# Optimization experiments

Hardware: AMD Instinct MI355X
Metric: run time of the kernel (lower is better)

## Reference

```python
import jax, jax.numpy as jnp
import numpy as np

FP8_MAX = 448.0  # max finite value of float8_e4m3fn


def setup_inputs() -> dict:
    key = jax.random.key(0)
    k1, k2, k3 = jax.random.split(key, 3)
    B, S, D_IN, D_OUT = 2, 4096, 2048, 8192
    x = jax.random.normal(k1, (B, S, D_IN), dtype=jnp.float32)
    # Weight is stored pre-quantized in fp8 (per-tensor scale), layout (in, out)
    w_fp32 = jax.random.normal(k2, (D_IN, D_OUT), dtype=jnp.float32) * 0.02
    weight_scale = jnp.float32(jnp.max(jnp.abs(w_fp32)) / FP8_MAX)
    weight = jnp.clip(w_fp32 / weight_scale, -FP8_MAX, FP8_MAX).astype(jnp.float8_e4m3fn)
    input_scale = jnp.float32(0.05)  # static per-tensor activation scale
    bias = jax.random.normal(k3, (D_OUT,), dtype=jnp.float32)
    return {"x": x, "weight": weight, "weight_scale": weight_scale,
            "input_scale": input_scale, "bias": bias}


def reference(x, weight, weight_scale, input_scale, bias):
    # static_quantize_e4m3_per_tensor: q = cast_fp8(clip(x / s)), returns (q, s)
    q = jnp.clip(x / input_scale, -FP8_MAX, FP8_MAX).astype(jnp.float8_e4m3fn)
    q2d = q.reshape(-1, q.shape[-1]).astype(jnp.float32)  # [B*S, D_in]
    w = weight.astype(jnp.float32)                         # [D_in, D_out]
    # cublas_scaled_mm: (q @ w) * scale_a * scale_b, out in x.dtype
    out = jnp.matmul(q2d, w) * (input_scale * weight_scale)
    out = out.astype(x.dtype) + bias.astype(x.dtype)
    return out.reshape(x.shape[:-1] + (out.shape[-1],))
```

## Files before the change

### kernel.cpp

```cpp
#include <hip/hip_runtime.h>

typedef __attribute__((ext_vector_type(4)))  float floatx4;
typedef __attribute__((ext_vector_type(16))) float floatx16;
typedef __attribute__((ext_vector_type(8)))  int   intx8;

__device__ __forceinline__ unsigned int pack4_fp8(float f0, float f1, float f2, float f3) {
    int v = __builtin_amdgcn_cvt_pk_fp8_f32(f0, f1, 0, false);
    v = __builtin_amdgcn_cvt_pk_fp8_f32(f2, f3, v, true);
    return (unsigned int)v;
}

__device__ __forceinline__ void gload16(const unsigned char* g, unsigned char* l) {
    __builtin_amdgcn_global_load_lds(
        (const __attribute__((address_space(1))) unsigned int*)g,
        (__attribute__((address_space(3))) unsigned int*)l, 16, 0, 0);
}

__global__ void detect_kernel(const unsigned int* __restrict__ W, int* __restrict__ flag) {
    __shared__ int ok[2];
    if (threadIdx.x == 0) { ok[0] = 1; ok[1] = 1; }
    __syncthreads();
    int f32ok = 1, bf16ok = 1;
#pragma unroll
    for (int i = 0; i < 16; ++i) {
        unsigned int w = W[threadIdx.x * 16 + i];
        if (w & 0x000FFFFFu) f32ok = 0;
        if (w & 0x000F000Fu) bf16ok = 0;
    }
    if (!f32ok)  atomicAnd(&ok[0], 0);
    if (!bf16ok) atomicAnd(&ok[1], 0);
    __syncthreads();
    if (threadIdx.x == 0) *flag = ok[0] ? 2 : (ok[1] ? 1 : 0);
}

__global__ void quant_kernel(const float* __restrict__ x,
                             unsigned int* __restrict__ q,
                             const float* __restrict__ iscale, int n8) {
    int i = blockIdx.x * blockDim.x + threadIdx.x;
    if (i >= n8) return;
    float s = iscale[0];
    const float4* xv = (const float4*)x;
    float4 a = xv[2 * i];
    float4 b = xv[2 * i + 1];
    float v[8] = {a.x, a.y, a.z, a.w, b.x, b.y, b.z, b.w};
#pragma unroll
    for (int j = 0; j < 8; ++j) {
        float t = v[j] / s;
        v[j] = fminf(fmaxf(t, -448.0f), 448.0f);
    }
    q[2 * i]     = pack4_fp8(v[0], v[1], v[2], v[3]);
    q[2 * i + 1] = pack4_fp8(v[4], v[5], v[6], v[7]);
}

template <int MODE>
__device__ __forceinline__ void ingest_body(const unsigned char* __restrict__ W,
                                            unsigned char* __restrict__ Wt,
                                            int K, int N,
                                            unsigned char (*tile)[68]) {
    const int k0 = blockIdx.y * 64;
    const int n0 = blockIdx.x * 64;
    const int t = threadIdx.x;
    const int kr = t >> 2;
    const int cg = (t & 3) * 16;
    const size_t eidx = (size_t)(k0 + kr) * N + (n0 + cg);

    unsigned int w4[4];
    if constexpr (MODE == 0) {
        uint4 v = *(const uint4*)(W + eidx);
        w4[0] = v.x; w4[1] = v.y; w4[2] = v.z; w4[3] = v.w;
    } else if constexpr (MODE == 1) {
        const uint4* p = (const uint4*)((const unsigned short*)W + eidx);
        uint4 A0 = p[0], A1 = p[1];
        unsigned int uw[8] = {A0.x, A0.y, A0.z, A0.w, A1.x, A1.y, A1.z, A1.w};
#pragma unroll
        for (int g = 0; g < 4; ++g) {
            float f0 = __uint_as_float((uw[2 * g] & 0xFFFFu) << 16);
            float f1 = __uint_as_float((uw[2 * g] >> 16) << 16);
            float f2 = __uint_as_float((uw[2 * g + 1] & 0xFFFFu) << 16);
            float f3 = __uint_as_float((uw[2 * g + 1] >> 16) << 16);
            w4[g] = pack4_fp8(f0, f1, f2, f3);
        }
    } else {
        const float4* p = (const float4*)((const float*)W + eidx);
#pragma unroll
        for (int g = 0; g < 4; ++g) {
            float4 f = p[g];
            w4[g] = pack4_fp8(f.x, f.y, f.z, f.w);
        }
    }
#pragma unroll
    for (int g = 0; g < 4; ++g)
        *(unsigned int*)&tile[kr][cg + 4 * g] = w4[g];
    __syncthreads();

    const int nr = t >> 2;
    const int kg = (t & 3) * 16;
    uint4 o;
    unsigned int w[4];
#pragma unroll
    for (int g = 0; g < 4; ++g) {
        unsigned int b0 = tile[kg + g * 4 + 0][nr];
        unsigned int b1 = tile[kg + g * 4 + 1][nr];
        unsigned int b2 = tile[kg + g * 4 + 2][nr];
        unsigned int b3 = tile[kg + g * 4 + 3][nr];
        w[g] = b0 | (b1 << 8) | (b2 << 16) | (b3 << 24);
    }
    o.x = w[0]; o.y = w[1]; o.z = w[2]; o.w = w[3];
    *(uint4*)(Wt + (size_t)(n0 + nr) * K + k0 + kg) = o;
}

__global__ void ingest_kernel(const unsigned char* __restrict__ W,
                              unsigned char* __restrict__ Wt,
                              const int* __restrict__ flag, int K, int N) {
    __shared__ __align__(16) unsigned char tile[64][68];
    const int mode = *flag;
    if (mode == 0)      ingest_body<0>(W, Wt, K, N, tile);
    else if (mode == 1) ingest_body<1>(W, Wt, K, N, tile);
    else                ingest_body<2>(W, Wt, K, N, tile);
}

__global__ __launch_bounds__(512, 2) void gemm_mxfp8_kernel(
    const unsigned char* __restrict__ A,
    const unsigned char* __restrict__ Bt,
    float* __restrict__ C,
    const float* __restrict__ bias,
    const float* __restrict__ wscale,
    const float* __restrict__ iscale,
    int M, int N, int K) {
    __shared__ __align__(16) unsigned char As[2 * 32768];
    __shared__ __align__(16) unsigned char Bs[2 * 32768];

    const int tid  = threadIdx.x;
    const int lane = tid & 63;
    const int wv   = tid >> 6;
    const int wm   = wv >> 2;
    const int wn   = wv & 3;
    const int r16  = lane & 15;
    const int cq   = lane >> 4;

    const int bm = blockIdx.y * 256;
    const int bn = blockIdx.x * 256;

    const unsigned char* ga[4];
    const unsigned char* gb[4];
    int lo[4];
#pragma unroll
    for (int j = 0; j < 4; ++j) {
        const int u   = wv * 4 + j;
        const int rb  = u >> 1;
        const int rg  = u & 1;
        const int row = rb * 16 + r16;
        const int col = cq * 32 + rg * 16;
        ga[j] = A  + (size_t)(bm + row) * K + col;
        gb[j] = Bt + (size_t)(bn + row) * K + col;
        lo[j] = u * 1024;
    }

    floatx16 acc[4][2] = {};
    const int NT = K >> 7;

    const int labase = ((lane >> 4) & 1) * 2048 + (lane & 15) * 16 + (lane >> 5) * 256;

#pragma unroll
    for (int j = 0; j < 4; ++j) {
        gload16(ga[j], &As[lo[j]]);
        gload16(gb[j], &Bs[lo[j]]);
        ga[j] += 128; gb[j] += 128;
    }
    if (NT > 1) {
#pragma unroll
        for (int j = 0; j < 4; ++j) {
            gload16(gb[j], &Bs[32768 + lo[j]]);
            gb[j] += 128;
        }
        asm volatile("s_waitcnt vmcnt(4)" ::: "memory");
    } else {
        asm volatile("s_waitcnt vmcnt(0)" ::: "memory");
    }
    __builtin_amdgcn_s_barrier();
    __builtin_amdgcn_sched_barrier(0);

    union U8 { intx8 v; uint4 q[2]; };

#define READ_FRAG(dst, p)                                           \
    do {                                                            \
        U8 _u;                                                      \
        _u.q[0] = *(const uint4*)(p);                               \
        _u.q[1] = *(const uint4*)((p) + 1024);                      \
        (dst) = _u.v;                                               \
    } while (0)

#define MFMA4(afA, afB, mA, mB, b0_, b1_)                                   \
    do {                                                                    \
        __builtin_amdgcn_s_setprio(1);                                      \
        acc[mA][0] = __builtin_amdgcn_mfma_scale_f32_32x32x64_f8f6f4(       \
            afA, b0_, acc[mA][0], 0, 0, 0, 0x7F7F7F7F, 0, 0x7F7F7F7F);      \
        acc[mA][1] = __builtin_amdgcn_mfma_scale_f32_32x32x64_f8f6f4(       \
            afA, b1_, acc[mA][1], 0, 0, 0, 0x7F7F7F7F, 0, 0x7F7F7F7F);      \
        acc[mB][0] = __builtin_amdgcn_mfma_scale_f32_32x32x64_f8f6f4(       \
            afB, b0_, acc[mB][0], 0, 0, 0, 0x7F7F7F7F, 0, 0x7F7F7F7F);      \
        acc[mB][1] = __builtin_amdgcn_mfma_scale_f32_32x32x64_f8f6f4(       \
            afB, b1_, acc[mB][1], 0, 0, 0, 0x7F7F7F7F, 0, 0x7F7F7F7F);      \
        __builtin_amdgcn_s_setprio(0);                                      \
    } while (0)

#define PHASE_WAIT()                                             \
    do {                                                         \
        __builtin_amdgcn_s_barrier();                            \
        asm volatile("s_waitcnt lgkmcnt(0)" ::: "memory");       \
        __builtin_amdgcn_sched_barrier(0);                       \
    } while (0)

    for (int kt = 0; kt < NT; ++kt) {
        const unsigned char* Ab = &As[(kt & 1) * 32768];
        const unsigned char* Bb = &Bs[(kt & 1) * 32768];
        unsigned char* An  = &As[((kt + 1) & 1) * 32768];
        unsigned char* Bn2 = &Bs[(kt & 1) * 32768];
        const bool pfA = (kt + 1 < NT);
        const bool pfB = (kt + 2 < NT);

        const unsigned char* aB = Ab + labase;
        const unsigned char* bB = Bb + labase;
        intx8 b00, b01, b10, b11, af0, af1;

        READ_FRAG(b00, bB + (wn * 4 + 0) * 2048);
        READ_FRAG(b01, bB + (wn * 4 + 2) * 2048);
        READ_FRAG(af0, aB + (wm * 8 + 0) * 2048);
        READ_FRAG(af1, aB + (wm * 8 + 2) * 2048);
        if (pfA) {
            gload16(ga[0], An + lo[0]); gload16(ga[1], An + lo[1]);
            ga[0] += 128; ga[1] += 128;
        }
        PHASE_WAIT();
        MFMA4(af0, af1, 0, 1, b00, b01);
        __builtin_amdgcn_s_barrier();

        READ_FRAG(b10, bB + (wn * 4 + 0) * 2048 + 512);
        READ_FRAG(b11, bB + (wn * 4 + 2) * 2048 + 512);
        READ_FRAG(af0, aB + (wm * 8 + 4) * 2048);
        READ_FRAG(af1, aB + (wm * 8 + 6) * 2048);
        if (pfA) {
            gload16(ga[2], An + lo[2]); gload16(ga[3], An + lo[3]);
            ga[2] += 128; ga[3] += 128;
        }
        PHASE_WAIT();
        MFMA4(af0, af1, 2, 3, b00, b01);
        __builtin_amdgcn_s_barrier();

        READ_FRAG(af0, aB + (wm * 8 + 0) * 2048 + 512);
        READ_FRAG(af1, aB + (wm * 8 + 2) * 2048 + 512);
        if (pfB) {
            gload16(gb[0], Bn2 + lo[0]); gload16(gb[1], Bn2 + lo[1]);
            gb[0] += 128; gb[1] += 128;
        }
        PHASE_WAIT();
        MFMA4(af0, af1, 0, 1, b10, b11);
        __builtin_amdgcn_s_barrier();

        READ_FRAG(af0, aB + (wm * 8 + 4) * 2048 + 512);
        READ_FRAG(af1, aB + (wm * 8 + 6) * 2048 + 512);
        if (pfB) {
            gload16(gb[2], Bn2 + lo[2]); gload16(gb[3], Bn2 + lo[3]);
            gb[2] += 128; gb[3] += 128;
        }
        PHASE_WAIT();
        MFMA4(af0, af1, 2, 3, b10, b11);
        if (pfB) {
            asm volatile("s_waitcnt vmcnt(4)" ::: "memory");
        } else {
            asm volatile("s_waitcnt vmcnt(0)" ::: "memory");
        }
        __builtin_amdgcn_s_barrier();
        __builtin_amdgcn_sched_barrier(0);
    }
    (void)M; (void)r16; (void)cq;
#undef READ_FRAG
#undef MFMA4
#undef PHASE_WAIT

    const float scale = iscale[0] * wscale[0];
    const int colb = bn + wn * 64 + (lane & 31);
    const float bv0 = bias[colb];
    const float bv1 = bias[colb + 32];
    const int rowb = bm + wm * 128 + 4 * (lane >> 5);
#pragma unroll
    for (int mb = 0; mb < 4; ++mb) {
#pragma unroll
        for (int r = 0; r < 16; ++r) {
            const int row = rowb + mb * 32 + (r & 3) + 8 * (r >> 2);
            float* cp = C + (size_t)row * N + colb;
            cp[0]  = acc[mb][0][r] * scale + bv0;
            cp[32] = acc[mb][1][r] * scale + bv1;
        }
    }
}

extern "C" void kernel_launch(void* const* d_in, const int* in_sizes, int n_in,
                              void* d_out, int out_size, void* d_ws, size_t ws_size,
                              hipStream_t stream) {
    const float* x          = (const float*)d_in[0];
    const unsigned char* w  = (const unsigned char*)d_in[1];
    const float* wscale     = (const float*)d_in[2];
    const float* iscale     = (const float*)d_in[3];
    const float* bias       = (const float*)d_in[4];
    float* out              = (float*)d_out;

    const int D_OUT = in_sizes[4];
    const int D_IN  = in_sizes[1] / D_OUT;
    const int M     = in_sizes[0] / D_IN;

    int* flag         = (int*)d_ws;
    unsigned char* q  = (unsigned char*)d_ws + 256;
    unsigned char* wt = q + (size_t)M * D_IN;

    detect_kernel<<<1, 256, 0, stream>>>((const unsigned int*)w, flag);
    const int n8 = (M * D_IN) / 8;
    quant_kernel<<<(n8 + 255) / 256, 256, 0, stream>>>(x, (unsigned int*)q, iscale, n8);
    dim3 tg(D_OUT / 64, D_IN / 64);
    ingest_kernel<<<tg, 256, 0, stream>>>(w, wt, flag, D_IN, D_OUT);
    gemm_mxfp8_kernel<<<dim3(D_OUT / 256, M / 256), 512, 0, stream>>>(
        q, wt, out, bias, wscale, iscale, M, D_OUT, D_IN);
}
```

Baseline: 507.4 us.

## Fuse prep kernels into one launch and halve GEMM K-tile depth

The detect, quantize and weight-ingest kernels are merged into one prep kernel. Blocks are split between activation quantization and weight transposition, and each ingest block now repeats the format detection itself, which removes two launches and the flag round-trip. The GEMM K-step drops from 128 to 64 bytes, halving shared-memory buffers to 64KB and cutting each iteration to two MFMA phases. This lowers LDS use and may raise occupancy, at the cost of twice as many barriers and loop iterations per unit of K.

Measured after the change: 503.5 us. Within noise of the previous version (-0.8%).

```diff
diff --git a/kernel.cpp b/kernel.cpp
--- a/kernel.cpp
+++ b/kernel.cpp
@@ -16,49 +16,11 @@
         (__attribute__((address_space(3))) unsigned int*)l, 16, 0, 0);
 }
 
-__global__ void detect_kernel(const unsigned int* __restrict__ W, int* __restrict__ flag) {
-    __shared__ int ok[2];
-    if (threadIdx.x == 0) { ok[0] = 1; ok[1] = 1; }
-    __syncthreads();
-    int f32ok = 1, bf16ok = 1;
-#pragma unroll
-    for (int i = 0; i < 16; ++i) {
-        unsigned int w = W[threadIdx.x * 16 + i];
-        if (w & 0x000FFFFFu) f32ok = 0;
-        if (w & 0x000F000Fu) bf16ok = 0;
-    }
-    if (!f32ok)  atomicAnd(&ok[0], 0);
-    if (!bf16ok) atomicAnd(&ok[1], 0);
-    __syncthreads();
-    if (threadIdx.x == 0) *flag = ok[0] ? 2 : (ok[1] ? 1 : 0);
-}
-
-__global__ void quant_kernel(const float* __restrict__ x,
-                             unsigned int* __restrict__ q,
-                             const float* __restrict__ iscale, int n8) {
-    int i = blockIdx.x * blockDim.x + threadIdx.x;
-    if (i >= n8) return;
-    float s = iscale[0];
-    const float4* xv = (const float4*)x;
-    float4 a = xv[2 * i];
-    float4 b = xv[2 * i + 1];
-    float v[8] = {a.x, a.y, a.z, a.w, b.x, b.y, b.z, b.w};
-#pragma unroll
-    for (int j = 0; j < 8; ++j) {
-        float t = v[j] / s;
-        v[j] = fminf(fmaxf(t, -448.0f), 448.0f);
-    }
-    q[2 * i]     = pack4_fp8(v[0], v[1], v[2], v[3]);
-    q[2 * i + 1] = pack4_fp8(v[4], v[5], v[6], v[7]);
-}
-
 template <int MODE>
 __device__ __forceinline__ void ingest_body(const unsigned char* __restrict__ W,
                                             unsigned char* __restrict__ Wt,
-                                            int K, int N,
+                                            int K, int N, int k0, int n0,
                                             unsigned char (*tile)[68]) {
-    const int k0 = blockIdx.y * 64;
-    const int n0 = blockIdx.x * 64;
     const int t = threadIdx.x;
     const int kr = t >> 2;
     const int cg = (t & 3) * 16;
@@ -109,14 +71,53 @@
     *(uint4*)(Wt + (size_t)(n0 + nr) * K + k0 + kg) = o;
 }
 
-__global__ void ingest_kernel(const unsigned char* __restrict__ W,
-                              unsigned char* __restrict__ Wt,
-                              const int* __restrict__ flag, int K, int N) {
+__global__ __launch_bounds__(256) void prep_kernel(
+    const float* __restrict__ x, unsigned int* __restrict__ q,
+    const float* __restrict__ iscale, int n8, int nbq,
+    const unsigned char* __restrict__ W, unsigned char* __restrict__ Wt,
+    int K, int N) {
+    __shared__ int ok[2];
     __shared__ __align__(16) unsigned char tile[64][68];
-    const int mode = *flag;
-    if (mode == 0)      ingest_body<0>(W, Wt, K, N, tile);
-    else if (mode == 1) ingest_body<1>(W, Wt, K, N, tile);
-    else                ingest_body<2>(W, Wt, K, N, tile);
+
+    if ((int)blockIdx.x < nbq) {
+        int i = blockIdx.x * 256 + threadIdx.x;
+        if (i >= n8) return;
+        float s = iscale[0];
+        const float4* xv = (const float4*)x;
+        float4 a = xv[2 * i];
+        float4 b = xv[2 * i + 1];
+        float v[8] = {a.x, a.y, a.z, a.w, b.x, b.y, b.z, b.w};
+#pragma unroll
+        for (int j = 0; j < 8; ++j) {
+            float t = v[j] / s;
+            v[j] = fminf(fmaxf(t, -448.0f), 448.0f);
+        }
+        q[2 * i]     = pack4_fp8(v[0], v[1], v[2], v[3]);
+        q[2 * i + 1] = pack4_fp8(v[4], v[5], v[6], v[7]);
+        return;
+    }
+
+    if (threadIdx.x == 0) { ok[0] = 1; ok[1] = 1; }
+    __syncthreads();
+    int f32ok = 1, bf16ok = 1;
+#pragma unroll
+    for (int i = 0; i < 16; ++i) {
+        unsigned int w = ((const unsigned int*)W)[threadIdx.x * 16 + i];
+        if (w & 0x000FFFFFu) f32ok = 0;
+        if (w & 0x000F000Fu) bf16ok = 0;
+    }
+    if (!f32ok)  atomicAnd(&ok[0], 0);
+    if (!bf16ok) atomicAnd(&ok[1], 0);
+    __syncthreads();
+    const int mode = ok[0] ? 2 : (ok[1] ? 1 : 0);
+
+    const int bx = blockIdx.x - nbq;
+    const int ntn = N >> 6;
+    const int n0 = (bx % ntn) * 64;
+    const int k0 = (bx / ntn) * 64;
+    if (mode == 0)      ingest_body<0>(W, Wt, K, N, k0, n0, tile);
+    else if (mode == 1) ingest_body<1>(W, Wt, K, N, k0, n0, tile);
+    else                ingest_body<2>(W, Wt, K, N, k0, n0, tile);
 }
 
 __global__ __launch_bounds__(512, 2) void gemm_mxfp8_kernel(
@@ -127,8 +128,8 @@
     const float* __restrict__ wscale,
     const float* __restrict__ iscale,
     int M, int N, int K) {
-    __shared__ __align__(16) unsigned char As[2 * 32768];
-    __shared__ __align__(16) unsigned char Bs[2 * 32768];
+    __shared__ __align__(16) unsigned char As[2 * 16384];
+    __shared__ __align__(16) unsigned char Bs[2 * 16384];
 
     const int tid  = threadIdx.x;
     const int lane = tid & 63;
@@ -141,39 +142,37 @@
     const int bm = blockIdx.y * 256;
     const int bn = blockIdx.x * 256;
 
-    const unsigned char* ga[4];
-    const unsigned char* gb[4];
-    int lo[4];
-#pragma unroll
-    for (int j = 0; j < 4; ++j) {
-        const int u   = wv * 4 + j;
-        const int rb  = u >> 1;
-        const int rg  = u & 1;
-        const int row = rb * 16 + r16;
-        const int col = cq * 32 + rg * 16;
+    const unsigned char* ga[2];
+    const unsigned char* gb[2];
+    int lo[2];
+#pragma unroll
+    for (int j = 0; j < 2; ++j) {
+        const int u   = wv * 2 + j;
+        const int row = u * 16 + r16;
+        const int col = cq * 16;
         ga[j] = A  + (size_t)(bm + row) * K + col;
         gb[j] = Bt + (size_t)(bn + row) * K + col;
         lo[j] = u * 1024;
     }
 
     floatx16 acc[4][2] = {};
-    const int NT = K >> 7;
-
-    const int labase = ((lane >> 4) & 1) * 2048 + (lane & 15) * 16 + (lane >> 5) * 256;
-
-#pragma unroll
-    for (int j = 0; j < 4; ++j) {
+    const int NT = K >> 6;
+
+    const int labase = ((lane >> 4) & 1) * 1024 + (lane & 15) * 16 + (lane >> 5) * 512;
+
+#pragma unroll
+    for (int j = 0; j < 2; ++j) {
         gload16(ga[j], &As[lo[j]]);
         gload16(gb[j], &Bs[lo[j]]);
-        ga[j] += 128; gb[j] += 128;
+        ga[j] += 64; gb[j] += 64;
     }
     if (NT > 1) {
 #pragma unroll
-        for (int j = 0; j < 4; ++j) {
-            gload16(gb[j], &Bs[32768 + lo[j]]);
-            gb[j] += 128;
-        }
-        asm volatile("s_waitcnt vmcnt(4)" ::: "memory");
+        for (int j = 0; j < 2; ++j) {
+            gload16(gb[j], &Bs[16384 + lo[j]]);
+            gb[j] += 64;
+        }
+        asm volatile("s_waitcnt vmcnt(2)" ::: "memory");
     } else {
         asm volatile("s_waitcnt vmcnt(0)" ::: "memory");
     }
@@ -186,7 +185,7 @@
     do {                                                            \
         U8 _u;                                                      \
         _u.q[0] = *(const uint4*)(p);                               \
-        _u.q[1] = *(const uint4*)((p) + 1024);                      \
+        _u.q[1] = *(const uint4*)((p) + 256);                       \
         (dst) = _u.v;                                               \
     } while (0)
 
@@ -212,68 +211,46 @@
     } while (0)
 
     for (int kt = 0; kt < NT; ++kt) {
-        const unsigned char* Ab = &As[(kt & 1) * 32768];
-        const unsigned char* Bb = &Bs[(kt & 1) * 32768];
-        unsigned char* An  = &As[((kt + 1) & 1) * 32768];
-        unsigned char* Bn2 = &Bs[(kt & 1) * 32768];
+        const unsigned char* Ab = &As[(kt & 1) * 16384];
+        const unsigned char* Bb = &Bs[(kt & 1) * 16384];
+        unsigned char* An  = &As[((kt + 1) & 1) * 16384];
+        unsigned char* Bn2 = &Bs[(kt & 1) * 16384];
         const bool pfA = (kt + 1 < NT);
         const bool pfB = (kt + 2 < NT);
 
         const unsigned char* aB = Ab + labase;
         const unsigned char* bB = Bb + labase;
-        intx8 b00, b01, b10, b11, af0, af1;
-
-        READ_FRAG(b00, bB + (wn * 4 + 0) * 2048);
-        READ_FRAG(b01, bB + (wn * 4 + 2) * 2048);
-        READ_FRAG(af0, aB + (wm * 8 + 0) * 2048);
-        READ_FRAG(af1, aB + (wm * 8 + 2) * 2048);
+        intx8 b0, b1, a0, a1;
+
+        READ_FRAG(b0, bB + (wn * 2 + 0) * 2048);
+        READ_FRAG(b1, bB + (wn * 2 + 1) * 2048);
+        READ_FRAG(a0, aB + (wm * 4 + 0) * 2048);
+        READ_FRAG(a1, aB + (wm * 4 + 1) * 2048);
         if (pfA) {
             gload16(ga[0], An + lo[0]); gload16(ga[1], An + lo[1]);
-            ga[0] += 128; ga[1] += 128;
+            ga[0] += 64; ga[1] += 64;
         }
         PHASE_WAIT();
-        MFMA4(af0, af1, 0, 1, b00, b01);
+        MFMA4(a0, a1, 0, 1, b0, b1);
         __builtin_amdgcn_s_barrier();
 
-        READ_FRAG(b10, bB + (wn * 4 + 0) * 2048 + 512);
-        READ_FRAG(b11, bB + (wn * 4 + 2) * 2048 + 512);
-        READ_FRAG(af0, aB + (wm * 8 + 4) * 2048);
-        READ_FRAG(af1, aB + (wm * 8 + 6) * 2048);
-        if (pfA) {
-            gload16(ga[2], An + lo[2]); gload16(ga[3], An + lo[3]);
-            ga[2] += 128; ga[3] += 128;
-        }
-        PHASE_WAIT();
-        MFMA4(af0, af1, 2, 3, b00, b01);
-        __builtin_amdgcn_s_barrier();
-
-        READ_FRAG(af0, aB + (wm * 8 + 0) * 2048 + 512);
-        READ_FRAG(af1, aB + (wm * 8 + 2) * 2048 + 512);
+        READ_FRAG(a0, aB + (wm * 4 + 2) * 2048);
+        READ_FRAG(a1, aB + (wm * 4 + 3) * 2048);
         if (pfB) {
             gload16(gb[0], Bn2 + lo[0]); gload16(gb[1], Bn2 + lo[1]);
-            gb[0] += 128; gb[1] += 128;
+            gb[0] += 64; gb[1] += 64;
         }
         PHASE_WAIT();
-        MFMA4(af0, af1, 0, 1, b10, b11);
-        __builtin_amdgcn_s_barrier();
-
-        READ_FRAG(af0, aB + (wm * 8 + 4) * 2048 + 512);
-        READ_FRAG(af1, aB + (wm * 8 + 6) * 2048 + 512);
+        MFMA4(a0, a1, 2, 3, b0, b1);
         if (pfB) {
-            gload16(gb[2], Bn2 + lo[2]); gload16(gb[3], Bn2 + lo[3]);
-            gb[2] += 128; gb[3] += 128;
-        }
-        PHASE_WAIT();
-        MFMA4(af0, af1, 2, 3, b10, b11);
-        if (pfB) {
-            asm volatile("s_waitcnt vmcnt(4)" ::: "memory");
+            asm volatile("s_waitcnt vmcnt(2)" ::: "memory");
         } else {
             asm volatile("s_waitcnt vmcnt(0)" ::: "memory");
         }
         __builtin_amdgcn_s_barrier();
         __builtin_amdgcn_sched_barrier(0);
     }
-    (void)M; (void)r16; (void)cq;
+    (void)M;
 #undef READ_FRAG
 #undef MFMA4
 #undef PHASE_WAIT
@@ -309,15 +286,14 @@
     const int D_IN  = in_sizes[1] / D_OUT;
     const int M     = in_sizes[0] / D_IN;
 
-    int* flag         = (int*)d_ws;
     unsigned char* q  = (unsigned char*)d_ws + 256;
     unsigned char* wt = q + (size_t)M * D_IN;
 
-    detect_kernel<<<1, 256, 0, stream>>>((const unsigned int*)w, flag);
-    const int n8 = (M * D_IN) / 8;
-    quant_kernel<<<(n8 + 255) / 256, 256, 0, stream>>>(x, (unsigned int*)q, iscale, n8);
-    dim3 tg(D_OUT / 64, D_IN / 64);
-    ingest_kernel<<<tg, 256, 0, stream>>>(w, wt, flag, D_IN, D_OUT);
+    const int n8  = (M * D_IN) / 8;
+    const int nbq = (n8 + 255) / 256;
+    const int nbi = (D_IN / 64) * (D_OUT / 64);
+    prep_kernel<<<nbq + nbi, 256, 0, stream>>>(
+        x, (unsigned int*)q, iscale, n8, nbq, w, wt, D_IN, D_OUT);
     gemm_mxfp8_kernel<<<dim3(D_OUT / 256, M / 256), 512, 0, stream>>>(
         q, wt, out, bias, wscale, iscale, M, D_OUT, D_IN);
 }
```
